# Kernel optimization log

Hardware: AMD Instinct MI355X
Metric: run time of the kernel (lower is better)

The kernel has to match this reference:

```python
import jax, jax.numpy as jnp
import numpy as np

B, N, E, D = 8, 2048, 4096, 256
HOPS = 3

def setup_inputs() -> dict:
    key = jax.random.key(0)
    ks = jax.random.split(key, 12)
    p = lambda k, shp: (jax.random.normal(k, shp, dtype=jnp.float32) * 0.02)
    return {
        "node_vec": jax.random.normal(ks[0], (B, N, D), dtype=jnp.float32),
        "edge_vec": jax.random.normal(ks[1], (B, E, D), dtype=jnp.float32),
        "node2edge": jax.random.uniform(ks[2], (B, E, N), dtype=jnp.float32),
        "edge2node": jax.random.uniform(ks[3], (B, N, E), dtype=jnp.float32),
        "node_mask": jnp.ones((B, N), dtype=jnp.float32),
        "W_fuse": p(ks[4], (D, 2 * D)), "b_fuse": jnp.zeros((D,), jnp.float32),
        "W_z": p(ks[5], (D, 4 * D)), "b_z": jnp.zeros((D,), jnp.float32),
        "W_update": p(ks[6], (D, 2 * D)),
        "W_reset": p(ks[7], (D, 2 * D)),
        "W_memory": p(ks[8], (D, 2 * D)),
        "W_max": p(ks[9], (D, D)),
    }

def _gnn_step(node_vec, edge_vec, n2e, e2n, W_fuse, b_fuse):
    # n2e: [B,E,N], e2n: [B,N,E]
    edge_emb = jnp.einsum('ben,bnd->bed', n2e, node_vec)          # [B,E,D]
    edge_emb = jax.nn.relu(jnp.concatenate([edge_emb, edge_vec], axis=-1) @ W_fuse.T + b_fuse)
    norm = jnp.sum(e2n, axis=2, keepdims=True) + 1.0               # [B,N,1]
    return (jnp.einsum('bne,bed->bnd', e2n, edge_emb) + node_vec) / norm

def _gated_fusion(in_vec, out_vec, W_z, b_z):
    feats = jnp.concatenate([in_vec, out_vec, in_vec * out_vec, in_vec - out_vec], axis=-1)
    z = jax.nn.sigmoid(feats @ W_z.T + b_z)
    return (1.0 - z) * in_vec + z * out_vec

def _gru_step(cur, new, W_u, W_r, W_m):
    cn = jnp.concatenate([cur, new], axis=-1)
    u = jax.nn.sigmoid(cn @ W_u.T)
    r = jax.nn.sigmoid(cn @ W_r.T)
    m = jnp.tanh(jnp.concatenate([r * cur, new], axis=-1) @ W_m.T)
    return (1.0 - u) * cur + u * m

def reference(node_vec, edge_vec, node2edge, edge2node, node_mask,
              W_fuse, b_fuse, W_z, b_z, W_update, W_reset, W_memory, W_max):
    n2e_T = jnp.swapaxes(node2edge, 1, 2)  # [B,N,E]
    e2n_T = jnp.swapaxes(edge2node, 1, 2)  # [B,E,N]
    for _ in range(HOPS):
        out_vec = _gnn_step(node_vec, edge_vec, node2edge, edge2node, W_fuse, b_fuse)
        in_vec = _gnn_step(node_vec, edge_vec, e2n_T, n2e_T, W_fuse, b_fuse)
        new_vec = _gated_fusion(in_vec, out_vec, W_z, b_z)
        node_vec = _gru_step(node_vec, new_vec, W_update, W_reset, W_memory)
    # graph max-pooling: linear then max over nodes (node_mask unused, as in original)
    graph_embedding = jnp.max(node_vec @ W_max.T, axis=1)          # [B,D]
    return (jnp.swapaxes(node_vec, 0, 1), graph_embedding[None])    # [N,B,D], [1,B,D]
```

## Files before the change

kernel.cpp:

```cpp
#include <hip/hip_runtime.h>
#include <math.h>

#define Bb 8
#define Nn 2048
#define Ee 4096
#define Dd 256
#define HOPS 3

typedef __attribute__((ext_vector_type(4))) float f32x4;
typedef _Float16 f16;
typedef __attribute__((ext_vector_type(8))) _Float16 f16x8;
typedef __attribute__((ext_vector_type(4))) _Float16 f16x4;
typedef __attribute__((ext_vector_type(8))) short s16x8;
typedef __attribute__((ext_vector_type(4))) short s16x4;

__device__ __forceinline__ short f2bf(float f){
  union{float f; unsigned u;} x; x.f=f;
  unsigned r = (x.u + 0x7fffu + ((x.u>>16)&1u)) >> 16;
  return (short)r;
}
__device__ __forceinline__ float bf2f(short h){
  union{unsigned u; float f;} x; x.u = ((unsigned)(unsigned short)h) << 16; return x.f;
}
__device__ __forceinline__ int swz(int row, int idx){ return idx ^ ((row & 7) << 3); }

enum { HN=0, HT=1 };
enum { OF=0, OH=1, OHT=2 };
enum { EP_NONE=0, EP_BIAS, EP_ADDRELUH, EP_AGG };
enum { SM_CN=0, SM_G4, SM_RC };
enum { SE_GATE=0, SE_SIG, SE_TANH };

__device__ __forceinline__ void xcd_remap(int& bx, int& by, int& bz) {
  const int nx = gridDim.x, ny = gridDim.y;
  const int nwg = nx * ny * gridDim.z;
  const int lin0 = blockIdx.x + nx * (blockIdx.y + ny * blockIdx.z);
  const int cpx = nwg >> 3;
  const int lin = (lin0 & 7) * cpx + (lin0 >> 3);
  bx = lin % nx;
  const int t1 = lin / nx;
  by = t1 % ny;
  bz = t1 / ny;
}

template<int AMODE, bool AH, int SPL, int EPI, int OUTM>
__global__ __launch_bounds__(512) void hgemm(
    const void* __restrict__ Av, const f16* __restrict__ Bh, void* __restrict__ Cv,
    const float* __restrict__ aux1, const float* __restrict__ aux2,
    const float* __restrict__ bias,
    int M, int Nd, int K, int lda, int ldb, int ldc,
    long sA, long sB, long sC, long sAux1, long sAux2,
    long aLo, long bLo, int maskB, int mask1)
{
  int bxi, byi, bz;
  xcd_remap(bxi, byi, bz);
  const char* Ab = (const char*)Av + (AH ? bz * sA * 2 : bz * sA * 4);
  Bh += (long)(bz & maskB) * sB;
  char* Cb = (char*)Cv + ((OUTM == OF) ? bz * sC * 4 : bz * sC * 2);
  if (aux1) aux1 += (long)(bz & mask1) * sAux1;
  if (aux2) aux2 += bz * sAux2;
  const int m0 = byi * 128;
  const int n0 = bxi * 128;

  constexpr int HLA = 128 * 64;
  constexpr int HLB = 128 * 64;
  __shared__ f16 As[128 * 64 * ((SPL & 2) ? 2 : 1)];
  __shared__ f16 Bs[128 * 64 * ((SPL & 1) ? 2 : 1)];

  const int tid = threadIdx.x;
  const int wid = tid >> 6, lane = tid & 63;
  const int wm = (wid >> 1) * 32, wn = (wid & 1) * 64;
  const int r = lane & 15, g = lane >> 4;

  f32x4 acc[2][4];
  #pragma unroll
  for (int i = 0; i < 2; i++)
    #pragma unroll
    for (int j = 0; j < 4; j++) acc[i][j] = (f32x4){0.f, 0.f, 0.f, 0.f};

  f16x8 ra0, ra1, rl0, rl1;
  f16x8 rb0, rb1, rbl0, rbl1;

  auto loadA = [&](int k0) {
    if (AMODE == HN && AH) {
      const f16* Ah = (const f16*)Ab;
      const int row = tid >> 2, kc = (tid & 3) * 16;
      const long off = (long)(m0 + row) * lda + k0 + kc;
      ra0 = *(const f16x8*)&Ah[off];
      ra1 = *(const f16x8*)&Ah[off + 8];
      if (SPL & 2) { rl0 = *(const f16x8*)&Ah[aLo + off]; rl1 = *(const f16x8*)&Ah[aLo + off + 8]; }
    } else if (AMODE == HN && !AH) {
      const float* Af = (const float*)Ab;
      const int row = tid >> 2, kc = (tid & 3) * 16;
      const float* s = &Af[(long)(m0 + row) * lda + k0 + kc];
      f32x4 v0 = *(const f32x4*)s,       v1 = *(const f32x4*)(s + 4);
      f32x4 v2 = *(const f32x4*)(s + 8), v3 = *(const f32x4*)(s + 12);
      ra0 = (f16x8){(f16)v0.x,(f16)v0.y,(f16)v0.z,(f16)v0.w,(f16)v1.x,(f16)v1.y,(f16)v1.z,(f16)v1.w};
      ra1 = (f16x8){(f16)v2.x,(f16)v2.y,(f16)v2.z,(f16)v2.w,(f16)v3.x,(f16)v3.y,(f16)v3.z,(f16)v3.w};
    } else {
      const int mm = tid & 127, kh = (tid >> 7) * 16;
      if (AH) {
        const f16* s = &((const f16*)Ab)[(long)(k0 + kh) * lda + m0 + mm];
        #pragma unroll
        for (int j = 0; j < 8; j++) ra0[j] = s[(long)j * lda];
        #pragma unroll
        for (int j = 0; j < 8; j++) ra1[j] = s[(long)(j + 8) * lda];
      } else {
        const float* s = &((const float*)Ab)[(long)(k0 + kh) * lda + m0 + mm];
        #pragma unroll
        for (int j = 0; j < 8; j++) ra0[j] = (f16)s[(long)j * lda];
        #pragma unroll
        for (int j = 0; j < 8; j++) ra1[j] = (f16)s[(long)(j + 8) * lda];
      }
    }
  };
  auto storeA = [&]() {
    if (AMODE == HT) {
      const int mm = tid & 127, kh = (tid >> 7) * 16;
      *(f16x8*)&As[swz(mm, mm * 64 + kh)]     = ra0;
      *(f16x8*)&As[swz(mm, mm * 64 + kh + 8)] = ra1;
    } else {
      const int row = tid >> 2, kc = (tid & 3) * 16;
      const int i0 = swz(row, row * 64 + kc), i1 = swz(row, row * 64 + kc + 8);
      *(f16x8*)&As[i0] = ra0;
      *(f16x8*)&As[i1] = ra1;
      if (SPL & 2) { *(f16x8*)&As[HLA + i0] = rl0; *(f16x8*)&As[HLA + i1] = rl1; }
    }
  };
  auto loadB = [&](int k0) {
    const int row = tid >> 2, kc = (tid & 3) * 16;
    const long off = (long)(n0 + row) * ldb + k0 + kc;
    rb0 = *(const f16x8*)&Bh[off];
    rb1 = *(const f16x8*)&Bh[off + 8];
    if (SPL & 1) { rbl0 = *(const f16x8*)&Bh[bLo + off]; rbl1 = *(const f16x8*)&Bh[bLo + off + 8]; }
  };
  auto storeB = [&]() {
    const int row = tid >> 2, kc = (tid & 3) * 16;
    const int i0 = swz(row, row * 64 + kc), i1 = swz(row, row * 64 + kc + 8);
    *(f16x8*)&Bs[i0] = rb0;
    *(f16x8*)&Bs[i1] = rb1;
    if (SPL & 1) { *(f16x8*)&Bs[HLB + i0] = rbl0; *(f16x8*)&Bs[HLB + i1] = rbl1; }
  };

  loadA(0); loadB(0);
  storeA(); storeB();
  __syncthreads();

  const int NT = K >> 6;
  for (int t = 0; t < NT; t++) {
    const bool more = (t + 1 < NT);
    if (more) { loadA((t + 1) << 6); loadB((t + 1) << 6); }
    #pragma unroll
    for (int ks = 0; ks < 2; ks++) {
      f16x8 af[2], bf[4], afl[2], bfl[4];
      #pragma unroll
      for (int i = 0; i < 2; i++) {
        const int rw = wm + i * 16 + r;
        const int ix = swz(rw, rw * 64 + ks * 32 + g * 8);
        af[i] = *(const f16x8*)&As[ix];
        if (SPL & 2) afl[i] = *(const f16x8*)&As[HLA + ix];
      }
      #pragma unroll
      for (int j = 0; j < 4; j++) {
        const int rw = wn + j * 16 + r;
        const int ix = swz(rw, rw * 64 + ks * 32 + g * 8);
        bf[j] = *(const f16x8*)&Bs[ix];
        if (SPL & 1) bfl[j] = *(const f16x8*)&Bs[HLB + ix];
      }
      #pragma unroll
      for (int i = 0; i < 2; i++)
        #pragma unroll
        for (int j = 0; j < 4; j++) {
          acc[i][j] = __builtin_amdgcn_mfma_f32_16x16x32_f16(af[i], bf[j], acc[i][j], 0, 0, 0);
          if (SPL & 1)
            acc[i][j] = __builtin_amdgcn_mfma_f32_16x16x32_f16(af[i], bfl[j], acc[i][j], 0, 0, 0);
          if (SPL & 2)
            acc[i][j] = __builtin_amdgcn_mfma_f32_16x16x32_f16(afl[i], bf[j], acc[i][j], 0, 0, 0);
        }
    }
    __syncthreads();
    if (more) { storeA(); storeB(); __syncthreads(); }
  }

  if (OUTM == OHT) {
    f16* tile = (f16*)Bs;
    #pragma unroll
    for (int half = 0; half < 2; half++) {
      __syncthreads();
      if ((wm >> 6) == half) {
        #pragma unroll
        for (int i = 0; i < 2; i++)
          #pragma unroll
          for (int j = 0; j < 4; j++) {
            const int rowl = wm + i * 16 + g * 4 - 64 * half;
            const int coll = wn + j * 16 + r;
            #pragma unroll
            for (int t = 0; t < 4; t++) {
              float v = acc[i][j][t];
              if (EPI == EP_ADDRELUH) {
                v += (float)((const f16*)aux1)[(long)(m0 + 64 * half + rowl + t) * 256 + n0 + coll];
                v = v > 0.f ? v : 0.f;
              } else if (EPI == EP_BIAS) { v += bias[n0 + coll]; }
              tile[coll * 72 + rowl + t] = (f16)v;
            }
          }
      }
      __syncthreads();
      const int c2 = tid >> 2, rs = (tid & 3) * 16;
      f16* dst = &((f16*)Cb)[(long)(n0 + c2) * ldc + m0 + 64 * half + rs];
      *(f16x8*)dst       = *(const f16x8*)&tile[c2 * 72 + rs];
      *(f16x8*)(dst + 8) = *(const f16x8*)&tile[c2 * 72 + rs + 8];
    }
  } else {
    #pragma unroll
    for (int i = 0; i < 2; i++) {
      #pragma unroll
      for (int j = 0; j < 4; j++) {
        const int rowb = m0 + wm + i * 16 + g * 4;
        const int col = n0 + wn + j * 16 + r;
        #pragma unroll
        for (int t = 0; t < 4; t++) {
          const int row = rowb + t;
          const long idx = (long)row * ldc + col;
          float v = acc[i][j][t];
          if (EPI == EP_BIAS)          { v += bias[col]; }
          else if (EPI == EP_ADDRELUH) { v += (float)((const f16*)aux1)[(long)row * 256 + col];
                                         v = v > 0.f ? v : 0.f; }
          else if (EPI == EP_AGG)      { v = (v + aux1[idx]) * aux2[row]; }
          if (OUTM == OH) ((f16*)Cb)[idx] = (f16)v;
          else            ((float*)Cb)[idx] = v;
        }
      }
    }
  }
}

template<int AMODE, int EPI>
__global__ __launch_bounds__(512) void ggemm(
    const float* __restrict__ A, const float* __restrict__ A2, const float* __restrict__ A3,
    const short* __restrict__ Bw, float* __restrict__ C,
    const float* __restrict__ aux1, const float* __restrict__ aux2, const float* __restrict__ bias,
    int Nd, int K, int lda, int ldb, int ldc, long bLo)
{
  int bxi, byi, bzu;
  xcd_remap(bxi, byi, bzu);
  const int m0 = byi * 128;
  const int n0 = bxi * 128;
  constexpr int HLA = 128 * 64;
  constexpr int HLB = 128 * 64;
  __shared__ short As[128 * 64 * 2];
  __shared__ short Bs[128 * 64 * 2];

  const int tid = threadIdx.x;
  const int wid = tid >> 6, lane = tid & 63;
  const int wm = (wid >> 1) * 32, wn = (wid & 1) * 64;
  const int r = lane & 15, g = lane >> 4;

  f32x4 acc[2][4];
  #pragma unroll
  for (int i = 0; i < 2; i++)
    #pragma unroll
    for (int j = 0; j < 4; j++) acc[i][j] = (f32x4){0.f, 0.f, 0.f, 0.f};

  s16x4 rah[4], ral[4];
  s16x8 rbh0, rbh1, rbl0, rbl1;

  auto loadA = [&](int k0) {
    const int row = tid >> 2, kc = (tid & 3) * 16;
    const int kk = k0 + kc, q = kk >> 8, kd = kk & 255;
    const long base = (long)(m0 + row) * 256 + kd;
    const long baseA = (long)(m0 + row) * lda + kd;
    #pragma unroll
    for (int u = 0; u < 4; u++) {
      f32x4 v;
      if (AMODE == SM_CN) {
        v = (q == 0) ? *(const f32x4*)(A + base + 4 * u)
                     : *(const f32x4*)(A2 + base + 4 * u);
      } else if (AMODE == SM_G4) {
        if (q == 0)      v = *(const f32x4*)(A  + base + 4 * u);
        else if (q == 1) v = *(const f32x4*)(A2 + base + 4 * u);
        else {
          f32x4 x = *(const f32x4*)(A  + base + 4 * u);
          f32x4 y = *(const f32x4*)(A2 + base + 4 * u);
          v = (q == 2) ? x * y : x - y;
        }
      } else {
        if (q == 0) {
          f32x4 x = *(const f32x4*)(A  + baseA + 4 * u);
          f32x4 y = *(const f32x4*)(A2 + base + 4 * u);
          v = x * y;
        } else v = *(const f32x4*)(A3 + base + 4 * u);
      }
      s16x4 h = { f2bf(v.x), f2bf(v.y), f2bf(v.z), f2bf(v.w) };
      rah[u] = h;
      ral[u] = (s16x4){ f2bf(v.x - bf2f(h.x)), f2bf(v.y - bf2f(h.y)),
                        f2bf(v.z - bf2f(h.z)), f2bf(v.w - bf2f(h.w)) };
    }
  };
  auto storeA = [&]() {
    const int row = tid >> 2, kc = (tid & 3) * 16;
    const int i0 = swz(row, row * 64 + kc), i1 = swz(row, row * 64 + kc + 8);
    *(s16x4*)&As[i0]     = rah[0]; *(s16x4*)&As[i0 + 4] = rah[1];
    *(s16x4*)&As[i1]     = rah[2]; *(s16x4*)&As[i1 + 4] = rah[3];
    *(s16x4*)&As[HLA + i0]     = ral[0]; *(s16x4*)&As[HLA + i0 + 4] = ral[1];
    *(s16x4*)&As[HLA + i1]     = ral[2]; *(s16x4*)&As[HLA + i1 + 4] = ral[3];
  };
  auto loadB = [&](int k0) {
    const int row = tid >> 2, kc = (tid & 3) * 16;
    const long off = (long)(n0 + row) * ldb + k0 + kc;
    rbh0 = *(const s16x8*)&Bw[off];
    rbh1 = *(const s16x8*)&Bw[off + 8];
    rbl0 = *(const s16x8*)&Bw[bLo + off];
    rbl1 = *(const s16x8*)&Bw[bLo + off + 8];
  };
  auto storeB = [&]() {
    const int row = tid >> 2, kc = (tid & 3) * 16;
    const int i0 = swz(row, row * 64 + kc), i1 = swz(row, row * 64 + kc + 8);
    *(s16x8*)&Bs[i0] = rbh0;
    *(s16x8*)&Bs[i1] = rbh1;
    *(s16x8*)&Bs[HLB + i0] = rbl0;
    *(s16x8*)&Bs[HLB + i1] = rbl1;
  };

  loadA(0); loadB(0);
  storeA(); storeB();
  __syncthreads();

  const int NT = K >> 6;
  for (int t = 0; t < NT; t++) {
    const bool more = (t + 1 < NT);
    if (more) { loadA((t + 1) << 6); loadB((t + 1) << 6); }
    #pragma unroll
    for (int ks = 0; ks < 2; ks++) {
      s16x8 ah[2], al[2], bh[4], bl[4];
      #pragma unroll
      for (int i = 0; i < 2; i++) {
        const int rw = wm + i * 16 + r;
        const int ix = swz(rw, rw * 64 + ks * 32 + g * 8);
        ah[i] = *(const s16x8*)&As[ix];
        al[i] = *(const s16x8*)&As[HLA + ix];
      }
      #pragma unroll
      for (int j = 0; j < 4; j++) {
        const int rw = wn + j * 16 + r;
        const int ix = swz(rw, rw * 64 + ks * 32 + g * 8);
        bh[j] = *(const s16x8*)&Bs[ix];
        bl[j] = *(const s16x8*)&Bs[HLB + ix];
      }
      #pragma unroll
      for (int i = 0; i < 2; i++)
        #pragma unroll
        for (int j = 0; j < 4; j++) {
          acc[i][j] = __builtin_amdgcn_mfma_f32_16x16x32_bf16(ah[i], bh[j], acc[i][j], 0, 0, 0);
          acc[i][j] = __builtin_amdgcn_mfma_f32_16x16x32_bf16(ah[i], bl[j], acc[i][j], 0, 0, 0);
          acc[i][j] = __builtin_amdgcn_mfma_f32_16x16x32_bf16(al[i], bh[j], acc[i][j], 0, 0, 0);
        }
    }
    __syncthreads();
    if (more) { storeA(); storeB(); __syncthreads(); }
  }

  #pragma unroll
  for (int i = 0; i < 2; i++) {
    #pragma unroll
    for (int j = 0; j < 4; j++) {
      #pragma unroll
      for (int t = 0; t < 4; t++) {
        const int row = m0 + wm + i * 16 + g * 4 + t;
        const int col = n0 + wn + j * 16 + r;
        float v = acc[i][j][t];
        if (EPI == SE_GATE) {
          v += bias[col];
          float z = 1.f / (1.f + __expf(-v));
          const long ix = (long)row * 256 + col;
          v = (1.f - z) * aux1[ix] + z * aux2[ix];
        } else if (EPI == SE_SIG) {
          v = 1.f / (1.f + __expf(-v));
        } else {
          v = tanhf(v);
        }
        C[(long)row * ldc + col] = v;
      }
    }
  }
}


template<bool SUMDST>
__global__ void cvt_dual(const float* __restrict__ in, f16* __restrict__ outR,
                         f16* __restrict__ outT, float* __restrict__ part, int R, int C) {
  __shared__ f16 t[64][72];
  __shared__ float sacc[64][4];
  const long boff = (long)blockIdx.z * (long)R * C;
  const int r0 = blockIdx.x * 64, c0 = blockIdx.y * 64;
  const int tid = threadIdx.x;
  const int rl = tid >> 2, cl = (tid & 3) * 16;
  const float* src = in + boff + (long)(r0 + rl) * C + c0 + cl;
  f16 loc[16];
  float s = 0.f;
  #pragma unroll
  for (int u = 0; u < 4; u++) {
    f32x4 v = *(const f32x4*)(src + 4 * u);
    loc[4*u+0] = (f16)v.x; loc[4*u+1] = (f16)v.y; loc[4*u+2] = (f16)v.z; loc[4*u+3] = (f16)v.w;
    if (!SUMDST) s += v.x + v.y + v.z + v.w;
  }
  f16* dR = outR + boff + (long)(r0 + rl) * C + c0 + cl;
  *(f16x8*)dR       = *(const f16x8*)&loc[0];
  *(f16x8*)(dR + 8) = *(const f16x8*)&loc[8];
  *(f16x8*)&t[rl][cl]     = *(const f16x8*)&loc[0];
  *(f16x8*)&t[rl][cl + 8] = *(const f16x8*)&loc[8];
  if (!SUMDST) sacc[rl][tid & 3] = s;
  __syncthreads();
  const int cl2 = tid >> 2, rl2 = (tid & 3) * 16;
  f16x8 o0, o1;
  #pragma unroll
  for (int v = 0; v < 8; v++) { o0[v] = t[rl2 + v][cl2]; o1[v] = t[rl2 + 8 + v][cl2]; }
  if (SUMDST) {
    float s2 = 0.f;
    #pragma unroll
    for (int v = 0; v < 8; v++) s2 += (float)o0[v] + (float)o1[v];
    sacc[cl2][tid & 3] = s2;
  }
  f16* dT = outT + boff + (long)(c0 + cl2) * R + r0 + rl2;
  *(f16x8*)dT = o0;
  *(f16x8*)(dT + 8) = o1;
  __syncthreads();
  if (tid < 64) {
    float tot = sacc[tid][0] + sacc[tid][1] + sacc[tid][2] + sacc[tid][3];
    const int slot = SUMDST ? blockIdx.x : blockIdx.y;
    const int n    = (SUMDST ? c0 : r0) + tid;
    part[((long)blockIdx.z * 64 + slot) * Nn + n] = tot;
  }
}

__global__ void colfin64(const float* __restrict__ part, float* __restrict__ rn) {
  const int i = blockIdx.x * 256 + threadIdx.x;
  const int b = i >> 11, n = i & 2047;
  float s = 0.f;
  for (int c = 0; c < 64; c++) s += part[((long)b * 64 + c) * Nn + n];
  rn[i] = 1.f / (1.f + s);
}

__global__ void rowsum_kernel(const float* __restrict__ e2n, float* __restrict__ out) {
  const int gw = blockIdx.x * 4 + (threadIdx.x >> 6);
  const int lane = threadIdx.x & 63;
  const float* p = e2n + (long)gw * Ee;
  float s = 0.f;
  for (int e = lane; e < Ee; e += 64) s += p[e];
  #pragma unroll
  for (int off = 32; off; off >>= 1) s += __shfl_down(s, off);
  if (lane == 0) out[gw] = 1.f / (1.f + s);
}
__global__ void colsum_kernel(const float* __restrict__ n2e, float* __restrict__ part) {
  const int n = blockIdx.x * 256 + threadIdx.x;
  const int c = blockIdx.y, b = blockIdx.z;
  const float* p = n2e + (long)b * Ee * Nn + (long)c * 256 * Nn + n;
  float s = 0.f;
  for (int e = 0; e < 256; e++) s += p[(long)e * Nn];
  part[((long)b * 16 + c) * Nn + n] = s;
}
__global__ void colfin16(const float* __restrict__ part, float* __restrict__ rni) {
  const int i = blockIdx.x * 256 + threadIdx.x;
  const int b = i >> 11, n = i & 2047;
  float s = 0.f;
  #pragma unroll
  for (int c = 0; c < 16; c++) s += part[((long)b * 16 + c) * Nn + n];
  rni[i] = 1.f / (1.f + s);
}

__global__ void cvt_half(const float* __restrict__ src, f16* __restrict__ dst) {
  const long i4 = (long)blockIdx.x * 256 + threadIdx.x;
  f32x4 v = *(const f32x4*)&src[i4 * 4];
  *(f16x4*)&dst[i4 * 4] = (f16x4){(f16)v.x, (f16)v.y, (f16)v.z, (f16)v.w};
}

__global__ void cvt_half_split(const float* __restrict__ src, f16* __restrict__ dst, long loOff) {
  const long i4 = (long)blockIdx.x * 256 + threadIdx.x;
  f32x4 v = *(const f32x4*)&src[i4 * 4];
  f16x4 h = {(f16)v.x, (f16)v.y, (f16)v.z, (f16)v.w};
  *(f16x4*)&dst[i4 * 4] = h;
  f16x4 l = {(f16)(v.x - (float)h[0]), (f16)(v.y - (float)h[1]),
             (f16)(v.z - (float)h[2]), (f16)(v.w - (float)h[3])};
  *(f16x4*)&dst[loOff + i4 * 4] = l;
}

__global__ void cvt_bf_split(const float* __restrict__ src, short* __restrict__ dst, long loOff) {
  const long i4 = (long)blockIdx.x * 256 + threadIdx.x;
  f32x4 v = *(const f32x4*)&src[i4 * 4];
  s16x4 h = { f2bf(v.x), f2bf(v.y), f2bf(v.z), f2bf(v.w) };
  *(s16x4*)&dst[i4 * 4] = h;
  s16x4 l = { f2bf(v.x - bf2f(h.x)), f2bf(v.y - bf2f(h.y)),
              f2bf(v.z - bf2f(h.z)), f2bf(v.w - bf2f(h.w)) };
  *(s16x4*)&dst[loOff + i4 * 4] = l;
}

__global__ void init_cur(const float* __restrict__ node_vec, float* __restrict__ cur,
                         f16* __restrict__ cur_h, long loOff) {
  const long i4 = (long)blockIdx.x * 256 + threadIdx.x;
  f32x4 v = *(const f32x4*)&node_vec[i4 * 4];
  *(f32x4*)&cur[i4 * 4] = v;
  f16x4 h = {(f16)v.x, (f16)v.y, (f16)v.z, (f16)v.w};
  *(f16x4*)&cur_h[i4 * 4] = h;
  f16x4 l = {(f16)(v.x - (float)h[0]), (f16)(v.y - (float)h[1]),
             (f16)(v.z - (float)h[2]), (f16)(v.w - (float)h[3])};
  *(f16x4*)&cur_h[loOff + i4 * 4] = l;
}

__global__ void transposeT(const float* __restrict__ cur, f16* __restrict__ curT, long loOff) {
  __shared__ f16 th[64][72];
  __shared__ f16 tl[64][72];
  const int b = blockIdx.z, nt = blockIdx.x * 64, dt = blockIdx.y * 64;
  const int tid = threadIdx.x;
  const int nl = tid >> 2, d0 = (tid & 3) * 16;
  const float* src = cur + ((long)b * Nn + nt + nl) * 256 + dt + d0;
  #pragma unroll
  for (int u = 0; u < 4; u++) {
    f32x4 v = *(const f32x4*)(src + 4 * u);
    f16x4 h = {(f16)v.x, (f16)v.y, (f16)v.z, (f16)v.w};
    *(f16x4*)&th[nl][d0 + 4 * u] = h;
    f16x4 l = {(f16)(v.x - (float)h[0]), (f16)(v.y - (float)h[1]),
               (f16)(v.z - (float)h[2]), (f16)(v.w - (float)h[3])};
    *(f16x4*)&tl[nl][d0 + 4 * u] = l;
  }
  __syncthreads();
  const int dl = tid >> 2, n0l = (tid & 3) * 16;
  f16x8 o0, o1, p0, p1;
  #pragma unroll
  for (int v = 0; v < 8; v++) {
    o0[v] = th[n0l + v][dl];     o1[v] = th[n0l + 8 + v][dl];
    p0[v] = tl[n0l + v][dl];     p1[v] = tl[n0l + 8 + v][dl];
  }
  f16* dst = curT + (long)b * (256 * Nn) + (long)(dt + dl) * Nn + nt + n0l;
  *(f16x8*)dst = o0;
  *(f16x8*)(dst + 8) = o1;
  *(f16x8*)(dst + loOff) = p0;
  *(f16x8*)(dst + loOff + 8) = p1;
}

__global__ void gruf_kernel(const float* __restrict__ urb, const float* __restrict__ m,
                            float* __restrict__ cur, f16* __restrict__ cur_h, long loOff) {
  const long i = (long)blockIdx.x * 256 + threadIdx.x;
  const long bn = i >> 8; const int d = i & 255;
  const float uu = urb[bn * 512 + d];
  const float v = (1.f - uu) * cur[i] + uu * m[i];
  cur[i] = v;
  f16 h = (f16)v;
  cur_h[i] = h;
  cur_h[loOff + i] = (f16)(v - (float)h);
}

__global__ void maxpool1(const float* __restrict__ pooled, float* __restrict__ part) {
  const int d = threadIdx.x, c = blockIdx.x, b = blockIdx.y;
  const float* p = pooled + ((long)b * Nn + c * 256) * Dd + d;
  float m = -INFINITY;
  for (int n = 0; n < 256; n++) m = fmaxf(m, p[(long)n * Dd]);
  part[(b * 8 + c) * Dd + d] = m;
}
__global__ void maxpool2(const float* __restrict__ part, float* __restrict__ out1) {
  const int d = threadIdx.x, b = blockIdx.x;
  float m = -INFINITY;
  #pragma unroll
  for (int c = 0; c < 8; c++) m = fmaxf(m, part[(b * 8 + c) * Dd + d]);
  out1[b * Dd + d] = m;
}
__global__ void transpose_out(const float* __restrict__ cur, float* __restrict__ out0) {
  const long i = (long)blockIdx.x * 256 + threadIdx.x;
  const int d = i & 255;
  const long nb = i >> 8;
  const int b = nb & 7;
  const long n = nb >> 3;
  out0[i] = cur[((long)b * Nn + n) * Dd + d];
}

extern "C" void kernel_launch(void* const* d_in, const int* in_sizes, int n_in,
                              void* d_out, int out_size, void* d_ws, size_t ws_size,
                              hipStream_t stream) {
  const float* node_vec = (const float*)d_in[0];
  const float* edge_vec = (const float*)d_in[1];
  const float* n2e      = (const float*)d_in[2];
  const float* e2n      = (const float*)d_in[3];
  const float* W_fuse   = (const float*)d_in[5];
  const float* b_fuse   = (const float*)d_in[6];
  const float* W_z      = (const float*)d_in[7];
  const float* b_z      = (const float*)d_in[8];
  const float* W_u      = (const float*)d_in[9];
  const float* W_r      = (const float*)d_in[10];
  const float* W_m      = (const float*)d_in[11];
  const float* W_max    = (const float*)d_in[12];

  const long ND  = (long)Bb * Nn * Dd;
  const long EDb = (long)Ee * Dd;
  const long NDb = (long)Nn * Dd;
  const long ED  = (long)Bb * EDb;
  const long ADJb = (long)Ee * Nn;
  const long ADJ = (long)Bb * ADJb;
  const int  BN  = Bb * Nn;

  char* p = (char*)d_ws;
  auto alloc = [&](size_t bytes) { char* r = p; p += (bytes + 255) & ~(size_t)255; return r; };

  const size_t need_full =
      (size_t)4 * ADJ * 2
      + (size_t)ED * 2
      + (size_t)4 * ED * 2
      + (size_t)ED * 2
      + (size_t)4 * ND * 2
      + (size_t)(2 * 131072 + 2 * 65536) * 2
      + (size_t)(2 * 262144 + 2 * 262144 + 2 * 131072) * 2
      + (size_t)5 * ND * 4
      + (size_t)BN * 512 * 4
      + (size_t)(2 * BN + 2 * 64 * BN) * 4
      + 64 * 1024;
  const bool full = ws_size >= need_full;

  f16 *adjEO = nullptr, *adjAG = nullptr;
  f16 *n2e_h = nullptr, *e2n_hT = nullptr, *e2n_h = nullptr, *n2e_hT = nullptr;
  if (full) {
    adjEO = (f16*)alloc((size_t)2 * ADJ * 2);
    adjAG = (f16*)alloc((size_t)2 * ADJ * 2);
    n2e_h = adjEO;  e2n_hT = adjEO + ADJ;
    e2n_h = adjAG;  n2e_hT = adjAG + ADJ;
  }
  f16* ev_h    = (f16*)alloc(ED * 2);
  f16* E1h2    = (f16*)alloc((size_t)2 * ED * 2);
  f16* E2T2    = (f16*)alloc((size_t)2 * ED * 2);
  f16* EVWh    = (f16*)alloc(ED * 2);
  f16* cur_h   = (f16*)alloc(2 * ND * 2);
  f16* cur_hT  = (f16*)alloc(2 * ND * 2);
  f16* Wf_h    = (f16*)alloc(2 * 131072 * 2);
  f16* Wmax_h  = (f16*)alloc(2 * 65536 * 2);
  short* Wz_s  = (short*)alloc((size_t)2 * 262144 * 2);
  short* Wur_s = (short*)alloc((size_t)2 * 262144 * 2);
  short* Wm_s  = (short*)alloc((size_t)2 * 131072 * 2);
  float* cur   = (float*)alloc(ND * 4);
  float* outv  = (float*)alloc(2 * ND * 4);
  float* inv   = outv + ND;
  float* nv    = (float*)alloc(ND * 4);
  float* urb   = (float*)alloc((size_t)BN * 512 * 4);
  float* mb    = (float*)alloc(ND * 4);
  float* rno   = (float*)alloc(2 * BN * 4);
  float* rni   = rno + BN;
  float* rnopart = (float*)alloc((size_t)64 * BN * 4);
  float* rnipart = (float*)alloc((size_t)64 * BN * 4);
  float* maxpart = (float*)alloc(BN * 4);

  float* out0 = (float*)d_out;
  float* out1 = out0 + ND;

  if (full) {
    cvt_dual<false><<<dim3(Nn / 64, Ee / 64, Bb), 256, 0, stream>>>(
        e2n, e2n_h, e2n_hT, rnopart, Nn, Ee);
    cvt_dual<true><<<dim3(Ee / 64, Nn / 64, Bb), 256, 0, stream>>>(
        n2e, n2e_h, n2e_hT, rnipart, Ee, Nn);
    colfin64<<<BN / 256, 256, 0, stream>>>(rnopart, rno);
    colfin64<<<BN / 256, 256, 0, stream>>>(rnipart, rni);
  } else {
    colsum_kernel<<<dim3(Nn / 256, 16, Bb), 256, 0, stream>>>(n2e, rnipart);
    colfin16<<<BN / 256, 256, 0, stream>>>(rnipart, rni);
    rowsum_kernel<<<BN / 4, 256, 0, stream>>>(e2n, rno);
  }
  cvt_half<<<(int)(ED / 1024), 256, 0, stream>>>(edge_vec, ev_h);
  cvt_half_split<<<131072 / 1024, 256, 0, stream>>>(W_fuse, Wf_h, 131072);
  cvt_half_split<<<65536 / 1024, 256, 0, stream>>>(W_max, Wmax_h, 65536);
  cvt_bf_split<<<262144 / 1024, 256, 0, stream>>>(W_z, Wz_s, 262144);
  cvt_bf_split<<<131072 / 1024, 256, 0, stream>>>(W_u, Wur_s, 262144);
  cvt_bf_split<<<131072 / 1024, 256, 0, stream>>>(W_r, Wur_s + 131072, 262144);
  cvt_bf_split<<<131072 / 1024, 256, 0, stream>>>(W_m, Wm_s, 131072);
  init_cur<<<(int)(ND / 1024), 256, 0, stream>>>(node_vec, cur, cur_h, ND);
  transposeT<<<dim3(Nn / 64, 4, Bb), 256, 0, stream>>>(cur, cur_hT, ND);

  hgemm<HN, true, 1, EP_BIAS, OH><<<dim3(2, Ee / 128, Bb), 512, 0, stream>>>(
      ev_h, Wf_h + 256, EVWh, nullptr, nullptr, b_fuse,
      Ee, 256, 256, 256, 512, 256, EDb, 0, EDb, 0, 0, 0, 131072, 0, 0);

  for (int h = 0; h < HOPS; h++) {
    if (full) {
      hgemm<HN, true, 1, EP_NONE, OH><<<dim3(2, Ee / 128, 2 * Bb), 512, 0, stream>>>(
          adjEO, cur_hT, E1h2, nullptr, nullptr, nullptr,
          Ee, 256, Nn, Nn, Nn, 256, ADJb, NDb, EDb, 0, 0, 0, ND, 7, 0);
      hgemm<HN, true, 1, EP_ADDRELUH, OHT><<<dim3(2, Ee / 128, 2 * Bb), 512, 0, stream>>>(
          E1h2, Wf_h, E2T2, (const float*)EVWh, nullptr, nullptr,
          Ee, 256, 256, 256, 512, Ee, EDb, 0, EDb, EDb / 2, 0, 0, 131072, 0, 7);
      hgemm<HN, true, 0, EP_AGG, OF><<<dim3(2, Nn / 128, 2 * Bb), 512, 0, stream>>>(
          adjAG, E2T2, outv, cur, rno, nullptr,
          Nn, 256, Ee, Ee, Ee, 256, ADJb, EDb, NDb, NDb, (long)Nn, 0, 0, 15, 7);
    } else {
      hgemm<HN, false, 1, EP_NONE, OH><<<dim3(2, Ee / 128, Bb), 512, 0, stream>>>(
          n2e, cur_hT, E1h2, nullptr, nullptr, nullptr,
          Ee, 256, Nn, Nn, Nn, 256, ADJb, NDb, EDb, 0, 0, 0, ND, 7, 0);
      hgemm<HT, false, 1, EP_NONE, OH><<<dim3(2, Ee / 128, Bb), 512, 0, stream>>>(
          e2n, cur_hT, E1h2 + ED, nullptr, nullptr, nullptr,
          Ee, 256, Nn, Ee, Nn, 256, ADJb, NDb, EDb, 0, 0, 0, ND, 7, 0);
      hgemm<HN, true, 1, EP_ADDRELUH, OHT><<<dim3(2, Ee / 128, 2 * Bb), 512, 0, stream>>>(
          E1h2, Wf_h, E2T2, (const float*)EVWh, nullptr, nullptr,
          Ee, 256, 256, 256, 512, Ee, EDb, 0, EDb, EDb / 2, 0, 0, 131072, 0, 7);
      hgemm<HN, false, 0, EP_AGG, OF><<<dim3(2, Nn / 128, Bb), 512, 0, stream>>>(
          e2n, E2T2, outv, cur, rno, nullptr,
          Nn, 256, Ee, Ee, Ee, 256, (long)Nn * Ee, EDb, NDb, NDb, (long)Nn, 0, 0, 15, 7);
      hgemm<HT, false, 0, EP_AGG, OF><<<dim3(2, Nn / 128, Bb), 512, 0, stream>>>(
          n2e, E2T2 + ED, inv, cur, rni, nullptr,
          Nn, 256, Ee, Nn, Ee, 256, (long)Ee * Nn, EDb, NDb, NDb, (long)Nn, 0, 0, 15, 7);
    }
    ggemm<SM_G4, SE_GATE><<<dim3(2, BN / 128, 1), 512, 0, stream>>>(
        inv, outv, nullptr, Wz_s, nv, inv, outv, b_z, 256, 1024, 256, 1024, 256, 262144);
    ggemm<SM_CN, SE_SIG><<<dim3(4, BN / 128, 1), 512, 0, stream>>>(
        cur, nv, nullptr, Wur_s, urb, nullptr, nullptr, nullptr, 512, 512, 256, 512, 512, 262144);
    ggemm<SM_RC, SE_TANH><<<dim3(2, BN / 128, 1), 512, 0, stream>>>(
        urb + 256, cur, nv, Wm_s, mb, nullptr, nullptr, nullptr, 256, 512, 512, 512, 256, 131072);
    gruf_kernel<<<(int)(ND / 256), 256, 0, stream>>>(urb, mb, cur, cur_h, ND);
    if (h < HOPS - 1)
      transposeT<<<dim3(Nn / 64, 4, Bb), 256, 0, stream>>>(cur, cur_hT, ND);
  }

  hgemm<HN, true, 3, EP_NONE, OF><<<dim3(2, BN / 128, 1), 512, 0, stream>>>(
      cur_h, Wmax_h, urb, nullptr, nullptr, nullptr,
      BN, 256, 256, 256, 256, 256, 0, 0, 0, 0, 0, ND, 65536, 0, 0);
  maxpool1<<<dim3(8, Bb), 256, 0, stream>>>(urb, maxpart);
  maxpool2<<<Bb, 256, 0, stream>>>(maxpart, out1);

  transpose_out<<<(int)(ND / 256), 256, 0, stream>>>(cur, out0);
}
```

Before: 1.591 ms.

## Fold W_z into three-block form and feed gate GEMMs pre-split bf16 operands

```diff
diff --git a/kernel.cpp b/kernel.cpp
--- a/kernel.cpp
+++ b/kernel.cpp
@@ -27,7 +27,7 @@
 enum { HN=0, HT=1 };
 enum { OF=0, OH=1, OHT=2 };
 enum { EP_NONE=0, EP_BIAS, EP_ADDRELUH, EP_AGG };
-enum { SM_CN=0, SM_G4, SM_RC };
+enum { GM_Z=0, GM_UR, GM_M };
 enum { SE_GATE=0, SE_SIG, SE_TANH };
 
 __device__ __forceinline__ void xcd_remap(int& bx, int& by, int& bz) {
@@ -49,13 +49,15 @@
     const float* __restrict__ bias,
     int M, int Nd, int K, int lda, int ldb, int ldc,
     long sA, long sB, long sC, long sAux1, long sAux2,
-    long aLo, long bLo, int maskB, int mask1)
+    long aLo, long bLo, int maskB, int mask1,
+    short* __restrict__ Cs, long csLo)
 {
   int bxi, byi, bz;
   xcd_remap(bxi, byi, bz);
   const char* Ab = (const char*)Av + (AH ? bz * sA * 2 : bz * sA * 4);
   Bh += (long)(bz & maskB) * sB;
   char* Cb = (char*)Cv + ((OUTM == OF) ? bz * sC * 4 : bz * sC * 2);
+  if (Cs) Cs += (long)bz * sC;
   if (aux1) aux1 += (long)(bz & mask1) * sAux1;
   if (aux2) aux2 += bz * sAux2;
   const int m0 = byi * 128;
@@ -228,6 +230,11 @@
           else if (EPI == EP_AGG)      { v = (v + aux1[idx]) * aux2[row]; }
           if (OUTM == OH) ((f16*)Cb)[idx] = (f16)v;
           else            ((float*)Cb)[idx] = v;
+          if (EPI == EP_AGG && Cs) {
+            short hh = f2bf(v);
+            Cs[idx] = hh;
+            Cs[csLo + idx] = f2bf(v - bf2f(hh));
+          }
         }
       }
     }
@@ -236,8 +243,10 @@
 
 template<int AMODE, int EPI>
 __global__ __launch_bounds__(512) void ggemm(
-    const float* __restrict__ A, const float* __restrict__ A2, const float* __restrict__ A3,
+    const float* __restrict__ A, const float* __restrict__ A2,
+    const short* __restrict__ P1, const short* __restrict__ P2, long pLo,
     const short* __restrict__ Bw, float* __restrict__ C,
+    short* __restrict__ Cs, long csLo,
     const float* __restrict__ aux1, const float* __restrict__ aux2, const float* __restrict__ bias,
     int Nd, int K, int lda, int ldb, int ldc, long bLo)
 {
@@ -261,48 +270,58 @@
     #pragma unroll
     for (int j = 0; j < 4; j++) acc[i][j] = (f32x4){0.f, 0.f, 0.f, 0.f};
 
-  s16x4 rah[4], ral[4];
+  s16x8 rh0, rh1, rlo0, rlo1;
   s16x8 rbh0, rbh1, rbl0, rbl1;
 
   auto loadA = [&](int k0) {
     const int row = tid >> 2, kc = (tid & 3) * 16;
-    const int kk = k0 + kc, q = kk >> 8, kd = kk & 255;
+    const int q = k0 >> 8, kd = (k0 + kc) & 255;
     const long base = (long)(m0 + row) * 256 + kd;
-    const long baseA = (long)(m0 + row) * lda + kd;
-    #pragma unroll
-    for (int u = 0; u < 4; u++) {
-      f32x4 v;
-      if (AMODE == SM_CN) {
-        v = (q == 0) ? *(const f32x4*)(A + base + 4 * u)
-                     : *(const f32x4*)(A2 + base + 4 * u);
-      } else if (AMODE == SM_G4) {
-        if (q == 0)      v = *(const f32x4*)(A  + base + 4 * u);
-        else if (q == 1) v = *(const f32x4*)(A2 + base + 4 * u);
-        else {
-          f32x4 x = *(const f32x4*)(A  + base + 4 * u);
-          f32x4 y = *(const f32x4*)(A2 + base + 4 * u);
-          v = (q == 2) ? x * y : x - y;
+    bool copy; const short* P;
+    if (AMODE == GM_Z)       { copy = (q < 2); P = (q == 0) ? P1 : P2; }
+    else if (AMODE == GM_UR) { copy = true;    P = (q == 0) ? P1 : P2; }
+    else                     { copy = (q == 1); P = P2; }
+    if (copy) {
+      rh0  = *(const s16x8*)&P[base];
+      rh1  = *(const s16x8*)&P[base + 8];
+      rlo0 = *(const s16x8*)&P[pLo + base];
+      rlo1 = *(const s16x8*)&P[pLo + base + 8];
+    } else {
+      float x[16];
+      if (AMODE == GM_Z) {
+        #pragma unroll
+        for (int u = 0; u < 4; u++) {
+          f32x4 a = *(const f32x4*)(A  + base + 4 * u);
+          f32x4 b = *(const f32x4*)(A2 + base + 4 * u);
+          f32x4 v = a * b;
+          x[4*u] = v.x; x[4*u+1] = v.y; x[4*u+2] = v.z; x[4*u+3] = v.w;
         }
       } else {
-        if (q == 0) {
-          f32x4 x = *(const f32x4*)(A  + baseA + 4 * u);
-          f32x4 y = *(const f32x4*)(A2 + base + 4 * u);
-          v = x * y;
-        } else v = *(const f32x4*)(A3 + base + 4 * u);
-      }
-      s16x4 h = { f2bf(v.x), f2bf(v.y), f2bf(v.z), f2bf(v.w) };
-      rah[u] = h;
-      ral[u] = (s16x4){ f2bf(v.x - bf2f(h.x)), f2bf(v.y - bf2f(h.y)),
-                        f2bf(v.z - bf2f(h.z)), f2bf(v.w - bf2f(h.w)) };
+        const long baseA = (long)(m0 + row) * lda + kd;
+        #pragma unroll
+        for (int u = 0; u < 4; u++) {
+          f32x4 a = *(const f32x4*)(A  + baseA + 4 * u);
+          f32x4 b = *(const f32x4*)(A2 + base + 4 * u);
+          f32x4 v = a * b;
+          x[4*u] = v.x; x[4*u+1] = v.y; x[4*u+2] = v.z; x[4*u+3] = v.w;
+        }
+      }
+      short hh[16], ll[16];
+      #pragma unroll
+      for (int e = 0; e < 16; e++) { hh[e] = f2bf(x[e]); ll[e] = f2bf(x[e] - bf2f(hh[e])); }
+      rh0  = (s16x8){hh[0],hh[1],hh[2],hh[3],hh[4],hh[5],hh[6],hh[7]};
+      rh1  = (s16x8){hh[8],hh[9],hh[10],hh[11],hh[12],hh[13],hh[14],hh[15]};
+      rlo0 = (s16x8){ll[0],ll[1],ll[2],ll[3],ll[4],ll[5],ll[6],ll[7]};
+      rlo1 = (s16x8){ll[8],ll[9],ll[10],ll[11],ll[12],ll[13],ll[14],ll[15]};
     }
   };
   auto storeA = [&]() {
     const int row = tid >> 2, kc = (tid & 3) * 16;
     const int i0 = swz(row, row * 64 + kc), i1 = swz(row, row * 64 + kc + 8);
-    *(s16x4*)&As[i0]     = rah[0]; *(s16x4*)&As[i0 + 4] = rah[1];
-    *(s16x4*)&As[i1]     = rah[2]; *(s16x4*)&As[i1 + 4] = rah[3];
-    *(s16x4*)&As[HLA + i0]     = ral[0]; *(s16x4*)&As[HLA + i0 + 4] = ral[1];
-    *(s16x4*)&As[HLA + i1]     = ral[2]; *(s16x4*)&As[HLA + i1 + 4] = ral[3];
+    *(s16x8*)&As[i0] = rh0;
+    *(s16x8*)&As[i1] = rh1;
+    *(s16x8*)&As[HLA + i0] = rlo0;
+    *(s16x8*)&As[HLA + i1] = rlo1;
   };
   auto loadB = [&](int k0) {
     const int row = tid >> 2, kc = (tid & 3) * 16;
@@ -367,6 +386,7 @@
       for (int t = 0; t < 4; t++) {
         const int row = m0 + wm + i * 16 + g * 4 + t;
         const int col = n0 + wn + j * 16 + r;
+        const long idx = (long)row * ldc + col;
         float v = acc[i][j][t];
         if (EPI == SE_GATE) {
           v += bias[col];
@@ -378,12 +398,29 @@
         } else {
           v = tanhf(v);
         }
-        C[(long)row * ldc + col] = v;
-      }
-    }
-  }
-}
-
+        C[idx] = v;
+        if (EPI == SE_GATE && Cs) {
+          short hh = f2bf(v);
+          Cs[idx] = hh;
+          Cs[csLo + idx] = f2bf(v - bf2f(hh));
+        }
+      }
+    }
+  }
+}
+
+
+__global__ void combine_wz(const float* __restrict__ Wz, short* __restrict__ Wc, long loOff) {
+  const int idx = blockIdx.x * 256 + threadIdx.x;
+  const int o = idx / 768, k = idx % 768;
+  float v;
+  if (k < 256)      v = Wz[o * 1024 + k] + Wz[o * 1024 + 768 + k];
+  else if (k < 512) v = Wz[o * 1024 + 256 + (k - 256)] - Wz[o * 1024 + 768 + (k - 256)];
+  else              v = Wz[o * 1024 + 512 + (k - 512)];
+  short h = f2bf(v);
+  Wc[idx] = h;
+  Wc[loOff + idx] = f2bf(v - bf2f(h));
+}
 
 template<bool SUMDST>
 __global__ void cvt_dual(const float* __restrict__ in, f16* __restrict__ outR,
@@ -494,7 +531,8 @@
 }
 
 __global__ void init_cur(const float* __restrict__ node_vec, float* __restrict__ cur,
-                         f16* __restrict__ cur_h, long loOff) {
+                         f16* __restrict__ cur_h, long loOff,
+                         short* __restrict__ cur_s, long sLo) {
   const long i4 = (long)blockIdx.x * 256 + threadIdx.x;
   f32x4 v = *(const f32x4*)&node_vec[i4 * 4];
   *(f32x4*)&cur[i4 * 4] = v;
@@ -503,6 +541,11 @@
   f16x4 l = {(f16)(v.x - (float)h[0]), (f16)(v.y - (float)h[1]),
              (f16)(v.z - (float)h[2]), (f16)(v.w - (float)h[3])};
   *(f16x4*)&cur_h[loOff + i4 * 4] = l;
+  s16x4 bh = { f2bf(v.x), f2bf(v.y), f2bf(v.z), f2bf(v.w) };
+  *(s16x4*)&cur_s[i4 * 4] = bh;
+  s16x4 bl = { f2bf(v.x - bf2f(bh.x)), f2bf(v.y - bf2f(bh.y)),
+               f2bf(v.z - bf2f(bh.z)), f2bf(v.w - bf2f(bh.w)) };
+  *(s16x4*)&cur_s[sLo + i4 * 4] = bl;
 }
 
 __global__ void transposeT(const float* __restrict__ cur, f16* __restrict__ curT, long loOff) {
@@ -537,7 +580,8 @@
 }
 
 __global__ void gruf_kernel(const float* __restrict__ urb, const float* __restrict__ m,
-                            float* __restrict__ cur, f16* __restrict__ cur_h, long loOff) {
+                            float* __restrict__ cur, f16* __restrict__ cur_h, long loOff,
+                            short* __restrict__ cur_s, long sLo) {
   const long i = (long)blockIdx.x * 256 + threadIdx.x;
   const long bn = i >> 8; const int d = i & 255;
   const float uu = urb[bn * 512 + d];
@@ -546,6 +590,9 @@
   f16 h = (f16)v;
   cur_h[i] = h;
   cur_h[loOff + i] = (f16)(v - (float)h);
+  short bh = f2bf(v);
+  cur_s[i] = bh;
+  cur_s[sLo + i] = f2bf(v - bf2f(bh));
 }
 
 __global__ void maxpool1(const float* __restrict__ pooled, float* __restrict__ part) {
@@ -606,9 +653,11 @@
       + (size_t)4 * ND * 2
       + (size_t)(2 * 131072 + 2 * 65536) * 2
       + (size_t)(2 * 262144 + 2 * 262144 + 2 * 131072) * 2
+      + (size_t)2 * 196608 * 2
       + (size_t)5 * ND * 4
       + (size_t)BN * 512 * 4
       + (size_t)(2 * BN + 2 * 64 * BN) * 4
+      + (size_t)(4 * ND + 2 * ND + 2 * ND) * 2
       + 64 * 1024;
   const bool full = ws_size >= need_full;
 
@@ -631,6 +680,7 @@
   short* Wz_s  = (short*)alloc((size_t)2 * 262144 * 2);
   short* Wur_s = (short*)alloc((size_t)2 * 262144 * 2);
   short* Wm_s  = (short*)alloc((size_t)2 * 131072 * 2);
+  short* Wzc_s = (short*)alloc((size_t)2 * 196608 * 2);
   float* cur   = (float*)alloc(ND * 4);
   float* outv  = (float*)alloc(2 * ND * 4);
   float* inv   = outv + ND;
@@ -642,6 +692,11 @@
   float* rnopart = (float*)alloc((size_t)64 * BN * 4);
   float* rnipart = (float*)alloc((size_t)64 * BN * 4);
   float* maxpart = (float*)alloc(BN * 4);
+  short* outinv_s = (short*)alloc((size_t)4 * ND * 2);
+  short* nv_s     = (short*)alloc((size_t)2 * ND * 2);
+  short* cur_s    = (short*)alloc((size_t)2 * ND * 2);
+  short* outv_s   = outinv_s;
+  short* inv_s    = outinv_s + ND;
 
   float* out0 = (float*)d_out;
   float* out1 = out0 + ND;
@@ -661,59 +716,65 @@
   cvt_half<<<(int)(ED / 1024), 256, 0, stream>>>(edge_vec, ev_h);
   cvt_half_split<<<131072 / 1024, 256, 0, stream>>>(W_fuse, Wf_h, 131072);
   cvt_half_split<<<65536 / 1024, 256, 0, stream>>>(W_max, Wmax_h, 65536);
-  cvt_bf_split<<<262144 / 1024, 256, 0, stream>>>(W_z, Wz_s, 262144);
+  combine_wz<<<196608 / 256, 256, 0, stream>>>(W_z, Wzc_s, 196608);
   cvt_bf_split<<<131072 / 1024, 256, 0, stream>>>(W_u, Wur_s, 262144);
   cvt_bf_split<<<131072 / 1024, 256, 0, stream>>>(W_r, Wur_s + 131072, 262144);
   cvt_bf_split<<<131072 / 1024, 256, 0, stream>>>(W_m, Wm_s, 131072);
-  init_cur<<<(int)(ND / 1024), 256, 0, stream>>>(node_vec, cur, cur_h, ND);
+  init_cur<<<(int)(ND / 1024), 256, 0, stream>>>(node_vec, cur, cur_h, ND, cur_s, ND);
   transposeT<<<dim3(Nn / 64, 4, Bb), 256, 0, stream>>>(cur, cur_hT, ND);
 
   hgemm<HN, true, 1, EP_BIAS, OH><<<dim3(2, Ee / 128, Bb), 512, 0, stream>>>(
       ev_h, Wf_h + 256, EVWh, nullptr, nullptr, b_fuse,
-      Ee, 256, 256, 256, 512, 256, EDb, 0, EDb, 0, 0, 0, 131072, 0, 0);
+      Ee, 256, 256, 256, 512, 256, EDb, 0, EDb, 0, 0, 0, 131072, 0, 0, nullptr, 0);
 
   for (int h = 0; h < HOPS; h++) {
     if (full) {
       hgemm<HN, true, 1, EP_NONE, OH><<<dim3(2, Ee / 128, 2 * Bb), 512, 0, stream>>>(
           adjEO, cur_hT, E1h2, nullptr, nullptr, nullptr,
-          Ee, 256, Nn, Nn, Nn, 256, ADJb, NDb, EDb, 0, 0, 0, ND, 7, 0);
+          Ee, 256, Nn, Nn, Nn, 256, ADJb, NDb, EDb, 0, 0, 0, ND, 7, 0, nullptr, 0);
       hgemm<HN, true, 1, EP_ADDRELUH, OHT><<<dim3(2, Ee / 128, 2 * Bb), 512, 0, stream>>>(
           E1h2, Wf_h, E2T2, (const float*)EVWh, nullptr, nullptr,
-          Ee, 256, 256, 256, 512, Ee, EDb, 0, EDb, EDb / 2, 0, 0, 131072, 0, 7);
+          Ee, 256, 256, 256, 512, Ee, EDb, 0, EDb, EDb / 2, 0, 0, 131072, 0, 7, nullptr, 0);
       hgemm<HN, true, 0, EP_AGG, OF><<<dim3(2, Nn / 128, 2 * Bb), 512, 0, stream>>>(
           adjAG, E2T2, outv, cur, rno, nullptr,
-          Nn, 256, Ee, Ee, Ee, 256, ADJb, EDb, NDb, NDb, (long)Nn, 0, 0, 15, 7);
+          Nn, 256, Ee, Ee, Ee, 256, ADJb, EDb, NDb, NDb, (long)Nn, 0, 0, 15, 7,
+          outinv_s, 2 * ND);
     } else {
       hgemm<HN, false, 1, EP_NONE, OH><<<dim3(2, Ee / 128, Bb), 512, 0, stream>>>(
           n2e, cur_hT, E1h2, nullptr, nullptr, nullptr,
-          Ee, 256, Nn, Nn, Nn, 256, ADJb, NDb, EDb, 0, 0, 0, ND, 7, 0);
+          Ee, 256, Nn, Nn, Nn, 256, ADJb, NDb, EDb, 0, 0, 0, ND, 7, 0, nullptr, 0);
       hgemm<HT, false, 1, EP_NONE, OH><<<dim3(2, Ee / 128, Bb), 512, 0, stream>>>(
           e2n, cur_hT, E1h2 + ED, nullptr, nullptr, nullptr,
-          Ee, 256, Nn, Ee, Nn, 256, ADJb, NDb, EDb, 0, 0, 0, ND, 7, 0);
+          Ee, 256, Nn, Ee, Nn, 256, ADJb, NDb, EDb, 0, 0, 0, ND, 7, 0, nullptr, 0);
       hgemm<HN, true, 1, EP_ADDRELUH, OHT><<<dim3(2, Ee / 128, 2 * Bb), 512, 0, stream>>>(
           E1h2, Wf_h, E2T2, (const float*)EVWh, nullptr, nullptr,
-          Ee, 256, 256, 256, 512, Ee, EDb, 0, EDb, EDb / 2, 0, 0, 131072, 0, 7);
+          Ee, 256, 256, 256, 512, Ee, EDb, 0, EDb, EDb / 2, 0, 0, 131072, 0, 7, nullptr, 0);
       hgemm<HN, false, 0, EP_AGG, OF><<<dim3(2, Nn / 128, Bb), 512, 0, stream>>>(
           e2n, E2T2, outv, cur, rno, nullptr,
-          Nn, 256, Ee, Ee, Ee, 256, (long)Nn * Ee, EDb, NDb, NDb, (long)Nn, 0, 0, 15, 7);
+          Nn, 256, Ee, Ee, Ee, 256, (long)Nn * Ee, EDb, NDb, NDb, (long)Nn, 0, 0, 15, 7,
+          outinv_s, 2 * ND);
       hgemm<HT, false, 0, EP_AGG, OF><<<dim3(2, Nn / 128, Bb), 512, 0, stream>>>(
           n2e, E2T2 + ED, inv, cur, rni, nullptr,
-          Nn, 256, Ee, Nn, Ee, 256, (long)Ee * Nn, EDb, NDb, NDb, (long)Nn, 0, 0, 15, 7);
-    }
-    ggemm<SM_G4, SE_GATE><<<dim3(2, BN / 128, 1), 512, 0, stream>>>(
-        inv, outv, nullptr, Wz_s, nv, inv, outv, b_z, 256, 1024, 256, 1024, 256, 262144);
-    ggemm<SM_CN, SE_SIG><<<dim3(4, BN / 128, 1), 512, 0, stream>>>(
-        cur, nv, nullptr, Wur_s, urb, nullptr, nullptr, nullptr, 512, 512, 256, 512, 512, 262144);
-    ggemm<SM_RC, SE_TANH><<<dim3(2, BN / 128, 1), 512, 0, stream>>>(
-        urb + 256, cur, nv, Wm_s, mb, nullptr, nullptr, nullptr, 256, 512, 512, 512, 256, 131072);
-    gruf_kernel<<<(int)(ND / 256), 256, 0, stream>>>(urb, mb, cur, cur_h, ND);
+          Nn, 256, Ee, Nn, Ee, 256, (long)Ee * Nn, EDb, NDb, NDb, (long)Nn, 0, 0, 15, 7,
+          outinv_s + ND, 2 * ND);
+    }
+    ggemm<GM_Z, SE_GATE><<<dim3(2, BN / 128, 1), 512, 0, stream>>>(
+        inv, outv, inv_s, outv_s, 2 * ND, Wzc_s, nv, nv_s, ND,
+        inv, outv, b_z, 256, 768, 256, 768, 256, 196608);
+    ggemm<GM_UR, SE_SIG><<<dim3(4, BN / 128, 1), 512, 0, stream>>>(
+        nullptr, nullptr, cur_s, nv_s, ND, Wur_s, urb, nullptr, 0,
+        nullptr, nullptr, nullptr, 512, 512, 0, 512, 512, 262144);
+    ggemm<GM_M, SE_TANH><<<dim3(2, BN / 128, 1), 512, 0, stream>>>(
+        urb + 256, cur, nullptr, nv_s, ND, Wm_s, mb, nullptr, 0,
+        nullptr, nullptr, nullptr, 256, 512, 512, 512, 256, 131072);
+    gruf_kernel<<<(int)(ND / 256), 256, 0, stream>>>(urb, mb, cur, cur_h, ND, cur_s, ND);
     if (h < HOPS - 1)
       transposeT<<<dim3(Nn / 64, 4, Bb), 256, 0, stream>>>(cur, cur_hT, ND);
   }
 
   hgemm<HN, true, 3, EP_NONE, OF><<<dim3(2, BN / 128, 1), 512, 0, stream>>>(
       cur_h, Wmax_h, urb, nullptr, nullptr, nullptr,
-      BN, 256, 256, 256, 256, 256, 0, 0, 0, 0, 0, ND, 65536, 0, 0);
+      BN, 256, 256, 256, 256, 256, 0, 0, 0, 0, 0, ND, 65536, 0, 0, nullptr, 0);
   maxpool1<<<dim3(8, Bb), 256, 0, stream>>>(urb, maxpart);
   maxpool2<<<Bb, 256, 0, stream>>>(maxpart, out1);
 
```

Result: no change. 1.568 ms (median of 2 runs) (-1.5%).
